# Kernel optimization log

Hardware: AMD Instinct MI355X
Metric: run time of the kernel (lower is better)

## Reference

```python
import jax, jax.numpy as jnp
import numpy as np

N = 50000      # nodes
E = 800000     # edges (avg degree 16)
R = 8          # relations
B = 30         # bases
EPS = 1e-5     # BatchNorm1d eps
ALPHA = 0.01   # LeakyReLU negative slope


def rgcn_conv(x, src, tgt, etype, basis, comp, root, bias):
    # PyG RGCNConv with basis decomposition, aggr='mean', flow=source_to_target.
    # W_r = sum_b comp[r,b] * basis[b]
    W = jnp.einsum('rb,bio->rio', comp, basis)          # [R, in, out]
    H = jnp.einsum('ni,rio->rno', x, W)                  # [R, N, out]
    m = H[etype, src]                                    # [E, out] per-edge messages
    # mean aggregation is per (target node, relation): divide by per-(tgt,rel) degree
    seg = tgt * R + etype                                # combined segment id
    deg = jax.ops.segment_sum(jnp.ones((src.shape[0],), x.dtype), seg,
                              num_segments=N * R)
    norm = 1.0 / jnp.maximum(deg, 1.0)
    m = m * norm[seg][:, None]
    agg = jax.ops.segment_sum(m, tgt, num_segments=N)    # [N, out]
    return agg + x @ root + bias


def batchnorm(x, gamma, beta):
    # training-mode BatchNorm1d: batch stats over node dim, biased variance
    mu = x.mean(axis=0)
    var = x.var(axis=0)
    return (x - mu) * jax.lax.rsqrt(var + EPS) * gamma + beta


def leaky_relu(x):
    return jnp.where(x > 0, x, ALPHA * x)


def setup_inputs() -> dict:
    key = jax.random.key(0)
    ks = jax.random.split(key, 12)
    s1 = 1.0 / np.sqrt(128.0)
    s2 = 1.0 / np.sqrt(256.0)
    s3 = 1.0 / np.sqrt(512.0)
    return {
        'embeddings': jax.random.normal(ks[0], (N, 128), jnp.float32),
        'edge_index': jax.random.randint(ks[1], (2, E), 0, N, jnp.int64
                                         if jax.config.jax_enable_x64 else jnp.int32),
        'edge_type': jax.random.randint(ks[2], (E,), 0, R, jnp.int64
                                        if jax.config.jax_enable_x64 else jnp.int32),
        'basis1': jax.random.normal(ks[3], (B, 128, 256), jnp.float32) * s1,
        'comp1': jax.random.normal(ks[4], (R, B), jnp.float32) * (1.0 / np.sqrt(B)),
        'root1': jax.random.normal(ks[5], (128, 256), jnp.float32) * s1,
        'bias1': jnp.zeros((256,), jnp.float32),
        'gamma1': jnp.ones((256,), jnp.float32),
        'beta1': jnp.zeros((256,), jnp.float32),
        'basis2': jax.random.normal(ks[6], (B, 256, 512), jnp.float32) * s2,
        'comp2': jax.random.normal(ks[7], (R, B), jnp.float32) * (1.0 / np.sqrt(B)),
        'root2': jax.random.normal(ks[8], (256, 512), jnp.float32) * s2,
        'bias2': jnp.zeros((512,), jnp.float32),
        'gamma2': jnp.ones((512,), jnp.float32),
        'beta2': jnp.zeros((512,), jnp.float32),
        'Wf': jax.random.normal(ks[9], (512, 512), jnp.float32) * s3,
        'bf': jnp.zeros((512,), jnp.float32),
    }


def reference(embeddings, edge_index, edge_type,
              basis1, comp1, root1, bias1, gamma1, beta1,
              basis2, comp2, root2, bias2, gamma2, beta2,
              Wf, bf):
    src, tgt = edge_index[0], edge_index[1]
    x = embeddings
    # layer 1: RGCNConv -> BN -> LeakyReLU (dropout = identity in eval)
    x = rgcn_conv(x, src, tgt, edge_type, basis1, comp1, root1, bias1)
    x = leaky_relu(batchnorm(x, gamma1, beta1))
    # layer 2
    x = rgcn_conv(x, src, tgt, edge_type, basis2, comp2, root2, bias2)
    x = leaky_relu(batchnorm(x, gamma2, beta2))
    # final reconstruction linear
    return x @ Wf + bf
```

## Files before the change

kernel.cpp:

```cpp
#include <hip/hip_runtime.h>
#include <hip/hip_bf16.h>

#define N_NODES 50000
#define N_EDGES 800000
#define R 8
#define NB 30
#define C1 128
#define C2 256
#define C3 512
#define NR (N_NODES * R)
#define BN_EPS 1e-5f
#define ALPHA 0.01f
#define XSTRIDE 1024

typedef unsigned short u16;
typedef __attribute__((ext_vector_type(8))) short short8;
typedef __attribute__((ext_vector_type(4))) float floatx4;

static inline unsigned cdivu(long long a, long long b) { return (unsigned)((a + b - 1) / b); }

__device__ __forceinline__ u16 f2bs(float f) {
    __hip_bfloat16 h = __float2bfloat16(f);
    return *reinterpret_cast<u16*>(&h);
}
__device__ __forceinline__ float b2f(u16 u) {
    return __uint_as_float(((unsigned)u) << 16);
}
__device__ __forceinline__ float ldacc(const float* p) { return *p; }
__device__ __forceinline__ float ldacc(const u16* p) { return b2f(*p); }
__device__ __forceinline__ void stv(float* p, float v) { *p = v; }
__device__ __forceinline__ void stv(u16* p, float v) { *p = f2bs(v); }

__device__ __forceinline__ void gl_lds16(const u16* g, u16* l) {
    __builtin_amdgcn_global_load_lds(
        (const __attribute__((address_space(1))) void*)g,
        (__attribute__((address_space(3))) void*)l, 16, 0, 0);
}

__global__ void k_b1(const float* __restrict__ comp, const float* __restrict__ basis,
                     const float* __restrict__ root, u16* __restrict__ Bt) {
    int t = blockIdx.x * blockDim.x + threadIdx.x;
    if (t >= C2 * 1152) return;
    int o = t % C2, k = t / C2;
    float v;
    if (k < R * C1) {
        int r = k >> 7, i = k & 127;
        v = 0.f;
        for (int b = 0; b < NB; ++b)
            v += comp[r * NB + b] * basis[((size_t)b * C1 + i) * C2 + o];
    } else v = root[(size_t)(k - R * C1) * C2 + o];
    Bt[(size_t)o * 1152 + k] = f2bs(v);
}
__global__ void k_b2(const float* __restrict__ comp, const float* __restrict__ basis,
                     const float* __restrict__ root, u16* __restrict__ Bt) {
    int t = blockIdx.x * blockDim.x + threadIdx.x;
    if (t >= C3 * 2304) return;
    int o = t % C3, k = t / C3;
    float v;
    if (k < R * C2) {
        int r = k >> 8, i = k & 255;
        v = 0.f;
        for (int b = 0; b < NB; ++b)
            v += comp[r * NB + b] * basis[((size_t)b * C2 + i) * C3 + o];
    } else v = root[(size_t)(k - R * C2) * C3 + o];
    Bt[(size_t)o * 2304 + k] = f2bs(v);
}
__global__ void k_btf(const float* __restrict__ Wf, u16* __restrict__ Bt) {
    int t = blockIdx.x * blockDim.x + threadIdx.x;
    if (t >= C3 * C3) return;
    int o = t % C3, k = t / C3;
    Bt[(size_t)o * C3 + k] = f2bs(Wf[(size_t)k * C3 + o]);
}

__global__ void k_f2b(const float* __restrict__ s, u16* __restrict__ d, long long n) {
    long long t = (long long)blockIdx.x * blockDim.x + threadIdx.x;
    if (t < n) d[t] = f2bs(s[t]);
}

__global__ void k_count(const int* __restrict__ tgt, const int* __restrict__ ety,
                        int* __restrict__ cnt) {
    int e = blockIdx.x * blockDim.x + threadIdx.x;
    if (e >= N_EDGES) return;
    atomicAdd(&cnt[tgt[e] * R + ety[e]], 1);
}
__global__ void k_scan1(const int* __restrict__ cnt, int* __restrict__ off,
                        int* __restrict__ bsum) {
    __shared__ int s[256];
    int tid = threadIdx.x;
    int i = blockIdx.x * 256 + tid;
    int v = (i < NR) ? cnt[i] : 0;
    s[tid] = v;
    __syncthreads();
    for (int o = 1; o < 256; o <<= 1) {
        int x = (tid >= o) ? s[tid - o] : 0;
        __syncthreads();
        s[tid] += x;
        __syncthreads();
    }
    if (i < NR) off[i] = s[tid] - v;
    if (tid == 255) bsum[blockIdx.x] = s[255];
}
__global__ void k_scan2(int* __restrict__ bsum, int nb) {
    __shared__ int s[256];
    __shared__ int carry_s;
    int tid = threadIdx.x;
    if (tid == 0) carry_s = 0;
    __syncthreads();
    for (int base = 0; base < nb; base += 256) {
        int i = base + tid;
        int v = (i < nb) ? bsum[i] : 0;
        s[tid] = v;
        __syncthreads();
        for (int o = 1; o < 256; o <<= 1) {
            int x = (tid >= o) ? s[tid - o] : 0;
            __syncthreads();
            s[tid] += x;
            __syncthreads();
        }
        int carry = carry_s;
        if (i < nb) bsum[i] = s[tid] - v + carry;
        int tot = s[255];
        __syncthreads();
        if (tid == 0) carry_s = carry + tot;
        __syncthreads();
    }
}
__global__ void k_scan3(int* __restrict__ off, const int* __restrict__ bsum,
                        int* __restrict__ cursor) {
    int i = blockIdx.x * 256 + threadIdx.x;
    if (i < NR) {
        int v = off[i] + bsum[blockIdx.x];
        off[i] = v;
        cursor[i] = v;
    }
    if (i == 0) off[NR] = N_EDGES;
}
__global__ void k_fill(const int* __restrict__ src, const int* __restrict__ tgt,
                       const int* __restrict__ ety, int* __restrict__ cursor,
                       int* __restrict__ esrc) {
    int e = blockIdx.x * blockDim.x + threadIdx.x;
    if (e >= N_EDGES) return;
    int pos = atomicAdd(&cursor[tgt[e] * R + ety[e]], 1);
    esrc[pos] = src[e];
}

template<int CIN, int NREL>
__global__ void k_gather(const int* __restrict__ off, const int* __restrict__ esrc,
                         const u16* __restrict__ srcbf, u16* __restrict__ Xbar, int r0) {
    constexpr int LPR = CIN / 8;
    constexpr int NSW = 64 / LPR;
    int wid = blockIdx.x * 4 + (threadIdx.x >> 6);
    if (wid >= N_NODES * NREL) return;
    int lane = threadIdx.x & 63;
    int sw = lane / LPR, l = lane & (LPR - 1);
    int t = wid / NREL, rr = wid - t * NREL;
    int b = t * R + r0 + rr;
    int o0 = off[b], o1 = off[b + 1];
    float acc[8] = {};
    for (int j = o0; j < o1; j += NSW) {
        int e = j + sw;
        if (e < o1) {
            int s = esrc[e];
            short8 v = *(const short8*)&srcbf[(size_t)s * CIN + l * 8];
            #pragma unroll
            for (int k = 0; k < 8; ++k) acc[k] += b2f((u16)v[k]);
        }
    }
    #pragma unroll
    for (int m = LPR; m < 64; m <<= 1)
        #pragma unroll
        for (int k = 0; k < 8; ++k) acc[k] += __shfl_xor(acc[k], m);
    int deg = o1 - o0;
    float w = (deg > 0) ? 1.f / (float)deg : 0.f;
    if (sw == 0) {
        short8 ov;
        #pragma unroll
        for (int k = 0; k < 8; ++k) ov[k] = (short)f2bs(acc[k] * w);
        *(short8*)&Xbar[(size_t)t * XSTRIDE + rr * CIN + l * 8] = ov;
    }
}

template<int CN, typename OT, bool ACC, bool BIAS, bool STATS>
__global__ __launch_bounds__(512, 2) void k_mgemm(
        const u16* __restrict__ A0, int sA0, int Ksplit,
        const u16* __restrict__ A1, int sA1, int Ktot,
        const u16* __restrict__ Bt, int sB,
        const float* __restrict__ bias, OT* __restrict__ C, int M,
        float* __restrict__ sumv, float* __restrict__ ssv) {
    extern __shared__ u16 lds[];
    u16* const Asl = lds;
    u16* const Bsl = lds + 32768;

    const int tid = threadIdx.x;
    const int lane = tid & 63, w = tid >> 6;
    const int wm = w >> 2, wn = w & 3;
    const int ml = lane & 15, qq = lane >> 4;
    const int ml7 = ml & 7;
    const int p0 = qq ^ ml7;
    const int p1 = (4 + qq) ^ ml7;
    const int aoff0 = (wm * 128 + ml) * 64 + p0 * 8;
    const int aoff1 = (wm * 128 + ml) * 64 + p1 * 8;
    const int boff0 = (wn * 64 + ml) * 64 + p0 * 8;
    const int boff1 = (wn * 64 + ml) * 64 + p1 * 8;

    const int nbx = gridDim.x;
    const int nwg = nbx * (int)gridDim.y;
    const int orig = blockIdx.y * nbx + blockIdx.x;
    const int qc = nwg >> 3, rc = nwg & 7;
    const int xcd = orig & 7, lin = orig >> 3;
    const int wgid = (xcd < rc ? xcd * (qc + 1) : rc * (qc + 1) + (xcd - rc) * qc) + lin;
    const int col0 = (wgid % nbx) * 256;
    const int row0 = (wgid / nbx) * 256;

    const int l8 = lane >> 3;
    const int csrc = ((lane & 7) ^ l8) * 8;
    const int rj0 = (2 * w + 0) * 8 + l8;
    const int rj1 = (2 * w + 1) * 8 + l8;
    const u16* A1g = A1 ? A1 : A0;
    const int  sA1g = A1 ? sA1 : sA0;
    int ga00 = row0 + rj0;        if (ga00 >= M) ga00 = M - 1;
    int ga01 = row0 + rj1;        if (ga01 >= M) ga01 = M - 1;
    int ga10 = row0 + 128 + rj0;  if (ga10 >= M) ga10 = M - 1;
    int ga11 = row0 + 128 + rj1;  if (ga11 >= M) ga11 = M - 1;
    const u16* pa00 = A0 + (size_t)ga00 * sA0 + csrc;
    const u16* pa01 = A0 + (size_t)ga01 * sA0 + csrc;
    const u16* pa10 = A0 + (size_t)ga10 * sA0 + csrc;
    const u16* pa11 = A0 + (size_t)ga11 * sA0 + csrc;
    const u16* ta00 = A1g + (size_t)ga00 * sA1g + csrc;
    const u16* ta01 = A1g + (size_t)ga01 * sA1g + csrc;
    const u16* ta10 = A1g + (size_t)ga10 * sA1g + csrc;
    const u16* ta11 = A1g + (size_t)ga11 * sA1g + csrc;
    const u16* pb00 = Bt + (size_t)(col0 + rj0) * sB + csrc;
    const u16* pb01 = Bt + (size_t)(col0 + rj1) * sB + csrc;
    const u16* pb10 = Bt + (size_t)(col0 + 128 + rj0) * sB + csrc;
    const u16* pb11 = Bt + (size_t)(col0 + 128 + rj1) * sB + csrc;

    const int dj0 = (2 * w + 0) * 512;
    const int dj1 = (2 * w + 1) * 512;

    const int NT = Ktot >> 6;
    const int ks64 = Ksplit >> 6;

    gl_lds16(pa00, Asl + dj0);          gl_lds16(pa01, Asl + dj1);          pa00 += 64; pa01 += 64;
    gl_lds16(pa10, Asl + 8192 + dj0);   gl_lds16(pa11, Asl + 8192 + dj1);   pa10 += 64; pa11 += 64;
    gl_lds16(pb00, Bsl + dj0);          gl_lds16(pb01, Bsl + dj1);          pb00 += 64; pb01 += 64;
    gl_lds16(pb10, Bsl + 8192 + dj0);   gl_lds16(pb11, Bsl + 8192 + dj1);   pb10 += 64; pb11 += 64;
    gl_lds16(pa00, Asl + 16384 + dj0);  gl_lds16(pa01, Asl + 16384 + dj1);  pa00 += 64; pa01 += 64;
    asm volatile("s_waitcnt vmcnt(2)" ::: "memory");
    __builtin_amdgcn_s_barrier();

    floatx4 acc[8][4] = {};
    short8 af[4][2], bfr[2][2];

    for (int t = 0; t < NT; ++t) {
        const int s = t & 1;
        u16* const As_s = Asl + s * 16384;
        u16* const Bs_s = Bsl + s * 16384;
        u16* const As_u = Asl + (s ^ 1) * 16384;
        u16* const Bs_u = Bsl + (s ^ 1) * 16384;
        if (t == ks64 - 1) { pa10 = ta10; pa11 = ta11; }
        if (t == ks64 - 2) { pa00 = ta00; pa01 = ta01; }
        const bool st1 = (t + 1 < NT), st2 = (t + 2 < NT);

        #pragma unroll
        for (int m = 0; m < 4; ++m) {
            af[m][0] = *(const short8*)(As_s + aoff0 + m * 1024);
            af[m][1] = *(const short8*)(As_s + aoff1 + m * 1024);
        }
        #pragma unroll
        for (int n = 0; n < 2; ++n) {
            bfr[n][0] = *(const short8*)(Bs_s + boff0 + n * 1024);
            bfr[n][1] = *(const short8*)(Bs_s + boff1 + n * 1024);
        }
        if (st1) { gl_lds16(pa10, As_u + 8192 + dj0); gl_lds16(pa11, As_u + 8192 + dj1);
                   pa10 += 64; pa11 += 64; }
        __builtin_amdgcn_s_barrier();
        asm volatile("s_waitcnt lgkmcnt(0)" ::: "memory");
        __builtin_amdgcn_sched_barrier(0);
        __builtin_amdgcn_s_setprio(1);
        #pragma unroll
        for (int m = 0; m < 4; ++m)
            #pragma unroll
            for (int n = 0; n < 2; ++n) {
                acc[m][n] = __builtin_amdgcn_mfma_f32_16x16x32_bf16(af[m][0], bfr[n][0], acc[m][n], 0, 0, 0);
                acc[m][n] = __builtin_amdgcn_mfma_f32_16x16x32_bf16(af[m][1], bfr[n][1], acc[m][n], 0, 0, 0);
            }
        __builtin_amdgcn_s_setprio(0);
        __builtin_amdgcn_s_barrier();

        #pragma unroll
        for (int n = 0; n < 2; ++n) {
            bfr[n][0] = *(const short8*)(Bs_s + boff0 + (2 + n) * 1024);
            bfr[n][1] = *(const short8*)(Bs_s + boff1 + (2 + n) * 1024);
        }
        if (st1) { gl_lds16(pb00, Bs_u + dj0); gl_lds16(pb01, Bs_u + dj1);
                   pb00 += 64; pb01 += 64; }
        __builtin_amdgcn_s_barrier();
        asm volatile("s_waitcnt lgkmcnt(0)" ::: "memory");
        __builtin_amdgcn_sched_barrier(0);
        __builtin_amdgcn_s_setprio(1);
        #pragma unroll
        for (int m = 0; m < 4; ++m)
            #pragma unroll
            for (int n = 0; n < 2; ++n) {
                acc[m][n + 2] = __builtin_amdgcn_mfma_f32_16x16x32_bf16(af[m][0], bfr[n][0], acc[m][n + 2], 0, 0, 0);
                acc[m][n + 2] = __builtin_amdgcn_mfma_f32_16x16x32_bf16(af[m][1], bfr[n][1], acc[m][n + 2], 0, 0, 0);
            }
        __builtin_amdgcn_s_setprio(0);
        __builtin_amdgcn_s_barrier();

        #pragma unroll
        for (int m = 0; m < 4; ++m) {
            af[m][0] = *(const short8*)(As_s + aoff0 + (4 + m) * 1024);
            af[m][1] = *(const short8*)(As_s + aoff1 + (4 + m) * 1024);
        }
        if (st1) { gl_lds16(pb10, Bs_u + 8192 + dj0); gl_lds16(pb11, Bs_u + 8192 + dj1);
                   pb10 += 64; pb11 += 64; }
        __builtin_amdgcn_s_barrier();
        asm volatile("s_waitcnt lgkmcnt(0)" ::: "memory");
        __builtin_amdgcn_sched_barrier(0);
        __builtin_amdgcn_s_setprio(1);
        #pragma unroll
        for (int m = 0; m < 4; ++m)
            #pragma unroll
            for (int n = 0; n < 2; ++n) {
                acc[4 + m][n + 2] = __builtin_amdgcn_mfma_f32_16x16x32_bf16(af[m][0], bfr[n][0], acc[4 + m][n + 2], 0, 0, 0);
                acc[4 + m][n + 2] = __builtin_amdgcn_mfma_f32_16x16x32_bf16(af[m][1], bfr[n][1], acc[4 + m][n + 2], 0, 0, 0);
            }
        __builtin_amdgcn_s_setprio(0);
        __builtin_amdgcn_s_barrier();

        #pragma unroll
        for (int n = 0; n < 2; ++n) {
            bfr[n][0] = *(const short8*)(Bs_s + boff0 + n * 1024);
            bfr[n][1] = *(const short8*)(Bs_s + boff1 + n * 1024);
        }
        if (st2) { gl_lds16(pa00, As_s + dj0); gl_lds16(pa01, As_s + dj1);
                   pa00 += 64; pa01 += 64; }
        __builtin_amdgcn_s_barrier();
        asm volatile("s_waitcnt lgkmcnt(0)" ::: "memory");
        __builtin_amdgcn_sched_barrier(0);
        __builtin_amdgcn_s_setprio(1);
        #pragma unroll
        for (int m = 0; m < 4; ++m)
            #pragma unroll
            for (int n = 0; n < 2; ++n) {
                acc[4 + m][n] = __builtin_amdgcn_mfma_f32_16x16x32_bf16(af[m][0], bfr[n][0], acc[4 + m][n], 0, 0, 0);
                acc[4 + m][n] = __builtin_amdgcn_mfma_f32_16x16x32_bf16(af[m][1], bfr[n][1], acc[4 + m][n], 0, 0, 0);
            }
        __builtin_amdgcn_s_setprio(0);
        asm volatile("s_waitcnt vmcnt(2)" ::: "memory");
        __builtin_amdgcn_s_barrier();
    }

    float cs[4] = {}, cq[4] = {};
    #pragma unroll
    for (int m = 0; m < 8; ++m) {
        #pragma unroll
        for (int rr = 0; rr < 4; ++rr) {
            int grow = row0 + wm * 128 + m * 16 + qq * 4 + rr;
            if (grow >= M) continue;
            #pragma unroll
            for (int n = 0; n < 4; ++n) {
                int gcol = col0 + wn * 64 + n * 16 + ml;
                float v = acc[m][n][rr];
                if (BIAS) v += bias[gcol];
                size_t idx = (size_t)grow * CN + gcol;
                if (ACC) v += ldacc(&C[idx]);
                if (STATS) { cs[n] += v; cq[n] += v * v; }
                stv(&C[idx], v);
            }
        }
    }
    if (STATS) {
        #pragma unroll
        for (int n = 0; n < 4; ++n) {
            float s = cs[n];
            s += __shfl_xor(s, 16); s += __shfl_xor(s, 32);
            float q2 = cq[n];
            q2 += __shfl_xor(q2, 16); q2 += __shfl_xor(q2, 32);
            if (lane < 16) {
                int gcol = col0 + wn * 64 + n * 16 + ml;
                atomicAdd(&sumv[gcol], s);
                atomicAdd(&ssv[gcol], q2);
            }
        }
    }
}

__global__ void k_bnprep(const float* __restrict__ sum, const float* __restrict__ ss,
                         const float* __restrict__ gamma, const float* __restrict__ beta,
                         float* __restrict__ scale, float* __restrict__ shift, int C) {
    int c = blockIdx.x * blockDim.x + threadIdx.x;
    if (c >= C) return;
    const float invN = 1.0f / (float)N_NODES;
    float mu = sum[c] * invN;
    float var = ss[c] * invN - mu * mu;
    float sc = rsqrtf(fmaxf(var, 0.f) + BN_EPS) * gamma[c];
    scale[c] = sc;
    shift[c] = beta[c] - mu * sc;
}

template<int C>
__global__ void k_bn8(u16* __restrict__ h, const float* __restrict__ scale,
                      const float* __restrict__ shift) {
    long long t = (long long)blockIdx.x * blockDim.x + threadIdx.x;
    if (t >= (long long)N_NODES * C / 8) return;
    long long base = t << 3;
    int c0 = (int)(base & (C - 1));
    short8 v = *(const short8*)&h[base];
    short8 o;
    #pragma unroll
    for (int k = 0; k < 8; ++k) {
        float y = b2f((u16)v[k]) * scale[c0 + k] + shift[c0 + k];
        o[k] = (short)f2bs(y > 0.f ? y : ALPHA * y);
    }
    *(short8*)&h[base] = o;
}

extern "C" void kernel_launch(void* const* d_in, const int* in_sizes, int n_in,
                              void* d_out, int out_size, void* d_ws, size_t ws_size,
                              hipStream_t stream) {
    const float* x      = (const float*)d_in[0];
    const int*   ei     = (const int*)d_in[1];
    const int*   ety    = (const int*)d_in[2];
    const float* basis1 = (const float*)d_in[3];
    const float* comp1  = (const float*)d_in[4];
    const float* root1  = (const float*)d_in[5];
    const float* bias1  = (const float*)d_in[6];
    const float* gamma1 = (const float*)d_in[7];
    const float* beta1  = (const float*)d_in[8];
    const float* basis2 = (const float*)d_in[9];
    const float* comp2  = (const float*)d_in[10];
    const float* root2  = (const float*)d_in[11];
    const float* bias2  = (const float*)d_in[12];
    const float* gamma2 = (const float*)d_in[13];
    const float* beta2  = (const float*)d_in[14];
    const float* Wf     = (const float*)d_in[15];
    const float* bf_    = (const float*)d_in[16];
    const int* src = ei;
    const int* tgt = ei + N_EDGES;

    static bool attr_done = false;
    if (!attr_done) {
        hipFuncSetAttribute((const void*)k_mgemm<C2, u16, false, true, true>,
                            hipFuncAttributeMaxDynamicSharedMemorySize, 131072);
        hipFuncSetAttribute((const void*)k_mgemm<C3, u16, false, true, false>,
                            hipFuncAttributeMaxDynamicSharedMemorySize, 131072);
        hipFuncSetAttribute((const void*)k_mgemm<C3, u16, true, false, true>,
                            hipFuncAttributeMaxDynamicSharedMemorySize, 131072);
        hipFuncSetAttribute((const void*)k_mgemm<C3, float, false, true, false>,
                            hipFuncAttributeMaxDynamicSharedMemorySize, 131072);
        attr_done = true;
    }

    const int nscanb = (NR + 255) / 256;
    char* p = (char*)d_ws;
    auto alloc = [&](size_t bytes) { void* r = (void*)p; p += (bytes + 63) & ~63ULL; return r; };
    u16* regionA = (u16*)alloc((size_t)N_NODES * XSTRIDE * 2);
    u16* h1bf    = (u16*)alloc((size_t)N_NODES * C2 * 2);
    u16* h2bf    = (u16*)alloc((size_t)N_NODES * C3 * 2);
    u16* xbf     = (u16*)alloc((size_t)N_NODES * C1 * 2);
    int* cnt     = (int*)alloc((size_t)NR * 4);
    int* off     = (int*)alloc((size_t)(NR + 1) * 4);
    int* cursor  = (int*)alloc((size_t)NR * 4);
    int* esrc    = (int*)alloc((size_t)N_EDGES * 4);
    int* bsum    = (int*)alloc((size_t)nscanb * 4);
    u16* Bt1     = (u16*)alloc((size_t)C2 * 1152 * 2);
    u16* Bt2     = (u16*)alloc((size_t)C3 * 2304 * 2);
    u16* Btf     = (u16*)alloc((size_t)C3 * C3 * 2);
    float* stats = (float*)alloc(3072 * 4);
    float* sum1 = stats, *ss1 = stats + 256, *sum2 = stats + 512, *ss2 = stats + 1024;
    float* sc1 = stats + 1536, *sh1 = stats + 1792;
    float* sc2 = stats + 2048, *sh2 = stats + 2560;

    hipMemsetAsync(cnt, 0, (size_t)NR * 4, stream);
    hipMemsetAsync(stats, 0, 1536 * 4, stream);

    k_b1<<<cdivu((long long)C2 * 1152, 256), 256, 0, stream>>>(comp1, basis1, root1, Bt1);
    k_b2<<<cdivu((long long)C3 * 2304, 256), 256, 0, stream>>>(comp2, basis2, root2, Bt2);
    k_btf<<<cdivu((long long)C3 * C3, 256), 256, 0, stream>>>(Wf, Btf);
    k_f2b<<<cdivu((long long)N_NODES * C1, 256), 256, 0, stream>>>(x, xbf, (long long)N_NODES * C1);
    k_count<<<cdivu(N_EDGES, 256), 256, 0, stream>>>(tgt, ety, cnt);
    k_scan1<<<nscanb, 256, 0, stream>>>(cnt, off, bsum);
    k_scan2<<<1, 256, 0, stream>>>(bsum, nscanb);
    k_scan3<<<nscanb, 256, 0, stream>>>(off, bsum, cursor);
    k_fill<<<cdivu(N_EDGES, 256), 256, 0, stream>>>(src, tgt, ety, cursor, esrc);

    const unsigned gym = cdivu(N_NODES, 256);

    k_gather<C1, 8><<<cdivu((long long)N_NODES * 8, 4), 256, 0, stream>>>(off, esrc, xbf, regionA, 0);
    {
        dim3 g(C2 / 256, gym);
        k_mgemm<C2, u16, false, true, true><<<g, 512, 131072, stream>>>(
            regionA, XSTRIDE, 1024, xbf, C1, 1152, Bt1, 1152, bias1, h1bf, N_NODES, sum1, ss1);
    }
    k_bnprep<<<1, C2, 0, stream>>>(sum1, ss1, gamma1, beta1, sc1, sh1, C2);
    k_bn8<C2><<<cdivu((long long)N_NODES * C2 / 8, 256), 256, 0, stream>>>(h1bf, sc1, sh1);

    {
        dim3 g(C3 / 256, gym);
        k_gather<C2, 4><<<cdivu((long long)N_NODES * 4, 4), 256, 0, stream>>>(off, esrc, h1bf, regionA, 0);
        k_mgemm<C3, u16, false, true, false><<<g, 512, 131072, stream>>>(
            regionA, XSTRIDE, 1024, (const u16*)nullptr, 0, 1024, Bt2, 2304, bias2, h2bf, N_NODES,
            nullptr, nullptr);
        k_gather<C2, 4><<<cdivu((long long)N_NODES * 4, 4), 256, 0, stream>>>(off, esrc, h1bf, regionA, 4);
        k_mgemm<C3, u16, true, false, true><<<g, 512, 131072, stream>>>(
            regionA, XSTRIDE, 1024, h1bf, C2, 1280, Bt2 + 1024, 2304, nullptr, h2bf, N_NODES,
            sum2, ss2);
    }
    k_bnprep<<<1, C3, 0, stream>>>(sum2, ss2, gamma2, beta2, sc2, sh2, C3);
    k_bn8<C3><<<cdivu((long long)N_NODES * C3 / 8, 256), 256, 0, stream>>>(h2bf, sc2, sh2);

    {
        dim3 g(C3 / 256, gym);
        k_mgemm<C3, float, false, true, false><<<g, 512, 131072, stream>>>(
            h2bf, C3, 512, (const u16*)nullptr, 0, 512, Btf, C3, bf_, (float*)d_out, N_NODES,
            nullptr, nullptr);
    }
}
```

Before: 791.3 us.

## Fuse neighbor mean-gather into GEMM A-tile staging, drop Xbar buffer

Removes the separate gather kernels and the intermediate per-relation aggregated buffer. The GEMM now builds each A tile itself: every thread walks the CSR edge list for its node and relation, averages the bf16 source rows, and writes the result straight into LDS instead of issuing an async global-to-LDS copy. This saves the write and re-read of a large intermediate buffer and several launches. In exchange, irregular, serialized edge loops now sit inside the MFMA pipeline with full vmcnt(0) waits. Each of the two column blocks also recomputes the same gather, so gather work is duplicated and the GEMM can stall behind memory latency.

```diff
diff --git a/kernel.cpp b/kernel.cpp
--- a/kernel.cpp
+++ b/kernel.cpp
@@ -11,7 +11,6 @@
 #define NR (N_NODES * R)
 #define BN_EPS 1e-5f
 #define ALPHA 0.01f
-#define XSTRIDE 1024
 
 typedef unsigned short u16;
 typedef __attribute__((ext_vector_type(8))) short short8;
@@ -144,49 +143,15 @@
     esrc[pos] = src[e];
 }
 
-template<int CIN, int NREL>
-__global__ void k_gather(const int* __restrict__ off, const int* __restrict__ esrc,
-                         const u16* __restrict__ srcbf, u16* __restrict__ Xbar, int r0) {
-    constexpr int LPR = CIN / 8;
-    constexpr int NSW = 64 / LPR;
-    int wid = blockIdx.x * 4 + (threadIdx.x >> 6);
-    if (wid >= N_NODES * NREL) return;
-    int lane = threadIdx.x & 63;
-    int sw = lane / LPR, l = lane & (LPR - 1);
-    int t = wid / NREL, rr = wid - t * NREL;
-    int b = t * R + r0 + rr;
-    int o0 = off[b], o1 = off[b + 1];
-    float acc[8] = {};
-    for (int j = o0; j < o1; j += NSW) {
-        int e = j + sw;
-        if (e < o1) {
-            int s = esrc[e];
-            short8 v = *(const short8*)&srcbf[(size_t)s * CIN + l * 8];
-            #pragma unroll
-            for (int k = 0; k < 8; ++k) acc[k] += b2f((u16)v[k]);
-        }
-    }
-    #pragma unroll
-    for (int m = LPR; m < 64; m <<= 1)
-        #pragma unroll
-        for (int k = 0; k < 8; ++k) acc[k] += __shfl_xor(acc[k], m);
-    int deg = o1 - o0;
-    float w = (deg > 0) ? 1.f / (float)deg : 0.f;
-    if (sw == 0) {
-        short8 ov;
-        #pragma unroll
-        for (int k = 0; k < 8; ++k) ov[k] = (short)f2bs(acc[k] * w);
-        *(short8*)&Xbar[(size_t)t * XSTRIDE + rr * CIN + l * 8] = ov;
-    }
-}
-
-template<int CN, typename OT, bool ACC, bool BIAS, bool STATS>
+template<int CN, typename OT, bool ACC, bool BIAS, bool STATS, bool GATHER, int CIN_LOG>
 __global__ __launch_bounds__(512, 2) void k_mgemm(
         const u16* __restrict__ A0, int sA0, int Ksplit,
         const u16* __restrict__ A1, int sA1, int Ktot,
         const u16* __restrict__ Bt, int sB,
         const float* __restrict__ bias, OT* __restrict__ C, int M,
-        float* __restrict__ sumv, float* __restrict__ ssv) {
+        float* __restrict__ sumv, float* __restrict__ ssv,
+        const int* __restrict__ off, const int* __restrict__ esrc,
+        const u16* __restrict__ gsrc, int R0) {
     extern __shared__ u16 lds[];
     u16* const Asl = lds;
     u16* const Bsl = lds + 32768;
@@ -214,39 +179,76 @@
 
     const int l8 = lane >> 3;
     const int csrc = ((lane & 7) ^ l8) * 8;
-    const int rj0 = (2 * w + 0) * 8 + l8;
-    const int rj1 = (2 * w + 1) * 8 + l8;
     const u16* A1g = A1 ? A1 : A0;
     const int  sA1g = A1 ? sA1 : sA0;
-    int ga00 = row0 + rj0;        if (ga00 >= M) ga00 = M - 1;
-    int ga01 = row0 + rj1;        if (ga01 >= M) ga01 = M - 1;
-    int ga10 = row0 + 128 + rj0;  if (ga10 >= M) ga10 = M - 1;
-    int ga11 = row0 + 128 + rj1;  if (ga11 >= M) ga11 = M - 1;
-    const u16* pa00 = A0 + (size_t)ga00 * sA0 + csrc;
-    const u16* pa01 = A0 + (size_t)ga01 * sA0 + csrc;
-    const u16* pa10 = A0 + (size_t)ga10 * sA0 + csrc;
-    const u16* pa11 = A0 + (size_t)ga11 * sA0 + csrc;
-    const u16* ta00 = A1g + (size_t)ga00 * sA1g + csrc;
-    const u16* ta01 = A1g + (size_t)ga01 * sA1g + csrc;
-    const u16* ta10 = A1g + (size_t)ga10 * sA1g + csrc;
-    const u16* ta11 = A1g + (size_t)ga11 * sA1g + csrc;
-    const u16* pb00 = Bt + (size_t)(col0 + rj0) * sB + csrc;
-    const u16* pb01 = Bt + (size_t)(col0 + rj1) * sB + csrc;
-    const u16* pb10 = Bt + (size_t)(col0 + 128 + rj0) * sB + csrc;
-    const u16* pb11 = Bt + (size_t)(col0 + 128 + rj1) * sB + csrc;
-
-    const int dj0 = (2 * w + 0) * 512;
-    const int dj1 = (2 * w + 1) * 512;
+    int gnode[2][2];
+    const u16* bA0[2][2];
+    const u16* bA1[2][2];
+    const u16* bB[2][2];
+    #pragma unroll
+    for (int h = 0; h < 2; ++h)
+        #pragma unroll
+        for (int c = 0; c < 2; ++c) {
+            int rj = (2 * w + c) * 8 + l8;
+            int ga = row0 + h * 128 + rj; if (ga >= M) ga = M - 1;
+            gnode[h][c] = ga;
+            bA0[h][c] = A0 + (size_t)ga * sA0 + csrc;
+            bA1[h][c] = A1g + (size_t)ga * sA1g + csrc;
+            bB[h][c]  = Bt + (size_t)(col0 + h * 128 + rj) * sB + csrc;
+        }
 
     const int NT = Ktot >> 6;
     const int ks64 = Ksplit >> 6;
 
-    gl_lds16(pa00, Asl + dj0);          gl_lds16(pa01, Asl + dj1);          pa00 += 64; pa01 += 64;
-    gl_lds16(pa10, Asl + 8192 + dj0);   gl_lds16(pa11, Asl + 8192 + dj1);   pa10 += 64; pa11 += 64;
-    gl_lds16(pb00, Bsl + dj0);          gl_lds16(pb01, Bsl + dj1);          pb00 += 64; pb01 += 64;
-    gl_lds16(pb10, Bsl + 8192 + dj0);   gl_lds16(pb11, Bsl + 8192 + dj1);   pb10 += 64; pb11 += 64;
-    gl_lds16(pa00, Asl + 16384 + dj0);  gl_lds16(pa01, Asl + 16384 + dj1);  pa00 += 64; pa01 += 64;
-    asm volatile("s_waitcnt vmcnt(2)" ::: "memory");
+    auto glA = [&](int ts, int h, u16* slot) {
+        const u16* a0 = (ts < ks64) ? bA0[h][0] + (size_t)ts * 64
+                                    : bA1[h][0] + (size_t)(ts - ks64) * 64;
+        const u16* a1 = (ts < ks64) ? bA0[h][1] + (size_t)ts * 64
+                                    : bA1[h][1] + (size_t)(ts - ks64) * 64;
+        gl_lds16(a0, slot + h * 8192 + (2 * w + 0) * 512);
+        gl_lds16(a1, slot + h * 8192 + (2 * w + 1) * 512);
+    };
+    auto glB = [&](int ts, int h, u16* slot) {
+        gl_lds16(bB[h][0] + (size_t)ts * 64, slot + h * 8192 + (2 * w + 0) * 512);
+        gl_lds16(bB[h][1] + (size_t)ts * 64, slot + h * 8192 + (2 * w + 1) * 512);
+    };
+    auto gstage = [&](int ts, int h, u16* slot) {
+        if constexpr (GATHER) {
+            const int rel = R0 + (ts >> (CIN_LOG - 6));
+            const int cb = (ts & ((1 << (CIN_LOG - 6)) - 1)) * 64 + csrc;
+            #pragma unroll
+            for (int c = 0; c < 2; ++c) {
+                const int seg = gnode[h][c] * R + rel;
+                const int o0 = off[seg], o1 = off[seg + 1];
+                float a[8] = {};
+                for (int j = o0; j < o1; ++j) {
+                    int s = esrc[j];
+                    short8 v = *(const short8*)(gsrc + ((size_t)s << CIN_LOG) + cb);
+                    #pragma unroll
+                    for (int k2 = 0; k2 < 8; ++k2) a[k2] += b2f((u16)v[k2]);
+                }
+                float wt = (o1 > o0) ? 1.f / (float)(o1 - o0) : 0.f;
+                short8 ov;
+                #pragma unroll
+                for (int k2 = 0; k2 < 8; ++k2) ov[k2] = (short)f2bs(a[k2] * wt);
+                *(short8*)(slot + h * 8192 + (2 * w + c) * 512 + lane * 8) = ov;
+            }
+        }
+    };
+
+    glB(0, 0, Bsl); glB(0, 1, Bsl);
+    {
+        u16* s0 = Asl; u16* s1 = Asl + 16384;
+        if (GATHER && 0 < ks64) gstage(0, 0, s0); else glA(0, 0, s0);
+        if (GATHER && 0 < ks64) gstage(0, 1, s0); else glA(0, 1, s0);
+        if (GATHER && 1 < ks64) gstage(1, 0, s1); else glA(1, 0, s1);
+    }
+    if constexpr (GATHER) {
+        asm volatile("s_waitcnt lgkmcnt(0)" ::: "memory");
+        asm volatile("s_waitcnt vmcnt(0)" ::: "memory");
+    } else {
+        asm volatile("s_waitcnt vmcnt(2)" ::: "memory");
+    }
     __builtin_amdgcn_s_barrier();
 
     floatx4 acc[8][4] = {};
@@ -258,9 +260,9 @@
         u16* const Bs_s = Bsl + s * 16384;
         u16* const As_u = Asl + (s ^ 1) * 16384;
         u16* const Bs_u = Bsl + (s ^ 1) * 16384;
-        if (t == ks64 - 1) { pa10 = ta10; pa11 = ta11; }
-        if (t == ks64 - 2) { pa00 = ta00; pa01 = ta01; }
         const bool st1 = (t + 1 < NT), st2 = (t + 2 < NT);
+        const bool g1 = GATHER && (t + 1) < ks64;
+        const bool g2 = GATHER && (t + 2) < ks64;
 
         #pragma unroll
         for (int m = 0; m < 4; ++m) {
@@ -272,8 +274,7 @@
             bfr[n][0] = *(const short8*)(Bs_s + boff0 + n * 1024);
             bfr[n][1] = *(const short8*)(Bs_s + boff1 + n * 1024);
         }
-        if (st1) { gl_lds16(pa10, As_u + 8192 + dj0); gl_lds16(pa11, As_u + 8192 + dj1);
-                   pa10 += 64; pa11 += 64; }
+        if (st1 && !g1) glA(t + 1, 1, As_u);
         __builtin_amdgcn_s_barrier();
         asm volatile("s_waitcnt lgkmcnt(0)" ::: "memory");
         __builtin_amdgcn_sched_barrier(0);
@@ -286,6 +287,10 @@
                 acc[m][n] = __builtin_amdgcn_mfma_f32_16x16x32_bf16(af[m][1], bfr[n][1], acc[m][n], 0, 0, 0);
             }
         __builtin_amdgcn_s_setprio(0);
+        if constexpr (GATHER) {
+            if (st1 && g1) gstage(t + 1, 1, As_u);
+            asm volatile("s_waitcnt lgkmcnt(0)" ::: "memory");
+        }
         __builtin_amdgcn_s_barrier();
 
         #pragma unroll
@@ -293,8 +298,7 @@
             bfr[n][0] = *(const short8*)(Bs_s + boff0 + (2 + n) * 1024);
             bfr[n][1] = *(const short8*)(Bs_s + boff1 + (2 + n) * 1024);
         }
-        if (st1) { gl_lds16(pb00, Bs_u + dj0); gl_lds16(pb01, Bs_u + dj1);
-                   pb00 += 64; pb01 += 64; }
+        if (st1) glB(t + 1, 0, Bs_u);
         __builtin_amdgcn_s_barrier();
         asm volatile("s_waitcnt lgkmcnt(0)" ::: "memory");
         __builtin_amdgcn_sched_barrier(0);
@@ -314,8 +318,7 @@
             af[m][0] = *(const short8*)(As_s + aoff0 + (4 + m) * 1024);
             af[m][1] = *(const short8*)(As_s + aoff1 + (4 + m) * 1024);
         }
-        if (st1) { gl_lds16(pb10, Bs_u + 8192 + dj0); gl_lds16(pb11, Bs_u + 8192 + dj1);
-                   pb10 += 64; pb11 += 64; }
+        if (st1) glB(t + 1, 1, Bs_u);
         __builtin_amdgcn_s_barrier();
         asm volatile("s_waitcnt lgkmcnt(0)" ::: "memory");
         __builtin_amdgcn_sched_barrier(0);
@@ -335,8 +338,7 @@
             bfr[n][0] = *(const short8*)(Bs_s + boff0 + n * 1024);
             bfr[n][1] = *(const short8*)(Bs_s + boff1 + n * 1024);
         }
-        if (st2) { gl_lds16(pa00, As_s + dj0); gl_lds16(pa01, As_s + dj1);
-                   pa00 += 64; pa01 += 64; }
+        if (st2 && !g2) glA(t + 2, 0, As_s);
         __builtin_amdgcn_s_barrier();
         asm volatile("s_waitcnt lgkmcnt(0)" ::: "memory");
         __builtin_amdgcn_sched_barrier(0);
@@ -349,7 +351,13 @@
                 acc[4 + m][n] = __builtin_amdgcn_mfma_f32_16x16x32_bf16(af[m][1], bfr[n][1], acc[4 + m][n], 0, 0, 0);
             }
         __builtin_amdgcn_s_setprio(0);
-        asm volatile("s_waitcnt vmcnt(2)" ::: "memory");
+        if constexpr (GATHER) {
+            if (st2 && g2) gstage(t + 2, 0, As_s);
+            asm volatile("s_waitcnt lgkmcnt(0)" ::: "memory");
+            asm volatile("s_waitcnt vmcnt(0)" ::: "memory");
+        } else {
+            asm volatile("s_waitcnt vmcnt(2)" ::: "memory");
+        }
         __builtin_amdgcn_s_barrier();
     }
 
@@ -375,13 +383,13 @@
     if (STATS) {
         #pragma unroll
         for (int n = 0; n < 4; ++n) {
-            float s = cs[n];
-            s += __shfl_xor(s, 16); s += __shfl_xor(s, 32);
+            float s2 = cs[n];
+            s2 += __shfl_xor(s2, 16); s2 += __shfl_xor(s2, 32);
             float q2 = cq[n];
             q2 += __shfl_xor(q2, 16); q2 += __shfl_xor(q2, 32);
             if (lane < 16) {
                 int gcol = col0 + wn * 64 + n * 16 + ml;
-                atomicAdd(&sumv[gcol], s);
+                atomicAdd(&sumv[gcol], s2);
                 atomicAdd(&ssv[gcol], q2);
             }
         }
@@ -443,13 +451,13 @@
 
     static bool attr_done = false;
     if (!attr_done) {
-        hipFuncSetAttribute((const void*)k_mgemm<C2, u16, false, true, true>,
+        hipFuncSetAttribute((const void*)k_mgemm<C2, u16, false, true, true, true, 7>,
                             hipFuncAttributeMaxDynamicSharedMemorySize, 131072);
-        hipFuncSetAttribute((const void*)k_mgemm<C3, u16, false, true, false>,
+        hipFuncSetAttribute((const void*)k_mgemm<C3, u16, false, true, false, true, 8>,
                             hipFuncAttributeMaxDynamicSharedMemorySize, 131072);
-        hipFuncSetAttribute((const void*)k_mgemm<C3, u16, true, false, true>,
+        hipFuncSetAttribute((const void*)k_mgemm<C3, u16, true, false, true, true, 8>,
                             hipFuncAttributeMaxDynamicSharedMemorySize, 131072);
-        hipFuncSetAttribute((const void*)k_mgemm<C3, float, false, true, false>,
+        hipFuncSetAttribute((const void*)k_mgemm<C3, float, false, true, false, false, 8>,
                             hipFuncAttributeMaxDynamicSharedMemorySize, 131072);
         attr_done = true;
     }
@@ -457,7 +465,6 @@
     const int nscanb = (NR + 255) / 256;
     char* p = (char*)d_ws;
     auto alloc = [&](size_t bytes) { void* r = (void*)p; p += (bytes + 63) & ~63ULL; return r; };
-    u16* regionA = (u16*)alloc((size_t)N_NODES * XSTRIDE * 2);
     u16* h1bf    = (u16*)alloc((size_t)N_NODES * C2 * 2);
     u16* h2bf    = (u16*)alloc((size_t)N_NODES * C3 * 2);
     u16* xbf     = (u16*)alloc((size_t)N_NODES * C1 * 2);
@@ -489,33 +496,31 @@
 
     const unsigned gym = cdivu(N_NODES, 256);
 
-    k_gather<C1, 8><<<cdivu((long long)N_NODES * 8, 4), 256, 0, stream>>>(off, esrc, xbf, regionA, 0);
     {
         dim3 g(C2 / 256, gym);
-        k_mgemm<C2, u16, false, true, true><<<g, 512, 131072, stream>>>(
-            regionA, XSTRIDE, 1024, xbf, C1, 1152, Bt1, 1152, bias1, h1bf, N_NODES, sum1, ss1);
+        k_mgemm<C2, u16, false, true, true, true, 7><<<g, 512, 131072, stream>>>(
+            xbf, C1, 1024, xbf, C1, 1152, Bt1, 1152, bias1, h1bf, N_NODES, sum1, ss1,
+            off, esrc, xbf, 0);
     }
     k_bnprep<<<1, C2, 0, stream>>>(sum1, ss1, gamma1, beta1, sc1, sh1, C2);
     k_bn8<C2><<<cdivu((long long)N_NODES * C2 / 8, 256), 256, 0, stream>>>(h1bf, sc1, sh1);
 
     {
         dim3 g(C3 / 256, gym);
-        k_gather<C2, 4><<<cdivu((long long)N_NODES * 4, 4), 256, 0, stream>>>(off, esrc, h1bf, regionA, 0);
-        k_mgemm<C3, u16, false, true, false><<<g, 512, 131072, stream>>>(
-            regionA, XSTRIDE, 1024, (const u16*)nullptr, 0, 1024, Bt2, 2304, bias2, h2bf, N_NODES,
-            nullptr, nullptr);
-        k_gather<C2, 4><<<cdivu((long long)N_NODES * 4, 4), 256, 0, stream>>>(off, esrc, h1bf, regionA, 4);
-        k_mgemm<C3, u16, true, false, true><<<g, 512, 131072, stream>>>(
-            regionA, XSTRIDE, 1024, h1bf, C2, 1280, Bt2 + 1024, 2304, nullptr, h2bf, N_NODES,
-            sum2, ss2);
+        k_mgemm<C3, u16, false, true, false, true, 8><<<g, 512, 131072, stream>>>(
+            h1bf, C2, 1024, h1bf, C2, 1024, Bt2, 2304, bias2, h2bf, N_NODES,
+            nullptr, nullptr, off, esrc, h1bf, 0);
+        k_mgemm<C3, u16, true, false, true, true, 8><<<g, 512, 131072, stream>>>(
+            h1bf, C2, 1024, h1bf, C2, 1280, Bt2 + 1024, 2304, nullptr, h2bf, N_NODES,
+            sum2, ss2, off, esrc, h1bf, 4);
     }
     k_bnprep<<<1, C3, 0, stream>>>(sum2, ss2, gamma2, beta2, sc2, sh2, C3);
     k_bn8<C3><<<cdivu((long long)N_NODES * C3 / 8, 256), 256, 0, stream>>>(h2bf, sc2, sh2);
 
     {
         dim3 g(C3 / 256, gym);
-        k_mgemm<C3, float, false, true, false><<<g, 512, 131072, stream>>>(
+        k_mgemm<C3, float, false, true, false, false, 8><<<g, 512, 131072, stream>>>(
             h2bf, C3, 512, (const u16*)nullptr, 0, 512, Btf, C3, bf_, (float*)d_out, N_NODES,
-            nullptr, nullptr);
-    }
-}
+            nullptr, nullptr, nullptr, nullptr, nullptr, 0);
+    }
+}
```

Measured after the change: 1.557 ms. 96.8% more time.
